# Kernel tuning notes

Measured on AMD Instinct MI355X. Metric: run time of the kernel, lower is better.

The kernel has to match this reference:

```python
import jax, jax.numpy as jnp
import numpy as np

NEG_SLOPE = 0.01  # torch nn.LeakyReLU default


def setup_inputs() -> dict:
    key = jax.random.key(0)
    k1, k2, k3, k4 = jax.random.split(key, 4)
    B, N, d = 256, 64, 64
    embeddings = jax.random.normal(k1, (B, N, d), dtype=jnp.float32)
    # nn.Linear(em_dim, em_dim): weight [d, d] (out, in), bias [d]
    w_W = jax.random.normal(k2, (d, d), dtype=jnp.float32) / np.sqrt(d)
    w_b = jax.random.normal(k3, (d,), dtype=jnp.float32) * 0.01
    # nn.Linear(em_dim, 1): weight [1, d] -> stored as [d], bias [1]
    a_W = jax.random.normal(k4, (d,), dtype=jnp.float32) / np.sqrt(d)
    a_b = jnp.zeros((1,), dtype=jnp.float32)
    return {"embeddings": embeddings, "w_W": w_W, "w_b": w_b, "a_W": a_W, "a_b": a_b}


def reference(embeddings, w_W, w_b, a_W, a_b):
    # pairwise elementwise product: value[b,i,j,d] = emb[b,i,d] * emb[b,j,d]
    value = embeddings[:, :, None, :] * embeddings[:, None, :, :]  # [B,N,N,d]
    # small linear d->d (torch Linear: x @ W.T + b)
    qk = jnp.einsum('bijd,ed->bije', value, w_W) + w_b
    qk = jnp.where(qk >= 0, qk, NEG_SLOPE * qk)  # LeakyReLU
    # dropout is identity in eval mode
    logits = jnp.einsum('bijd,d->bij', qk, a_W) + a_b[0]  # linear d->1, squeeze
    alphas = jax.nn.softmax(logits, axis=-1)[..., None]  # [B,N,N,1]
    return alphas, value
```

## Files before the change

kernel.cpp:

```cpp
#include <hip/hip_runtime.h>

typedef __attribute__((ext_vector_type(8))) short short8;
typedef __attribute__((ext_vector_type(4))) float floatx4;
typedef __attribute__((ext_vector_type(4))) int   intx4;

#define NEG_SLOPE 0.01f

__device__ __forceinline__ short f2bf(float f) {
    unsigned u = __float_as_uint(f);
    unsigned r = (u + 0x7FFFu + ((u >> 16) & 1u)) >> 16;
    return (short)r;
}

__device__ __forceinline__ int pack2(float x, float y) {
    return (int)(unsigned short)f2bf(x) | ((int)(unsigned short)f2bf(y) << 16);
}

__global__ __launch_bounds__(256, 2)
void afm_kernel(const float* __restrict__ emb,
                const float* __restrict__ wW,
                const float* __restrict__ wb,
                const float* __restrict__ aW,
                float* __restrict__ aOut,
                float* __restrict__ vOut) {
    __shared__ __align__(16) float sEf[64][68];
    __shared__ __align__(16) float sW [64][68];
    __shared__ __align__(16) short sEb[64][72];
    __shared__ __align__(16) float sei[4][64];
    __shared__ __align__(16) float swb[64];
    __shared__ __align__(16) float saw[64];
    __shared__ __align__(16) float slog[4][64];

    const int tid   = threadIdx.x;
    const int lane  = tid & 63;
    const int w     = tid >> 6;
    const int blk   = blockIdx.x;
    const int b     = blk >> 4;
    const int iBase = (blk & 15) << 2;
    const int i     = iBase + w;

    const float* embB = emb + (size_t)b * 4096;

    {
        int row = tid >> 2;
        int c0  = (tid & 3) << 4;
        const float* src = embB + row * 64 + c0;
        float4 a0 = *(const float4*)(src);
        float4 a1 = *(const float4*)(src + 4);
        float4 a2 = *(const float4*)(src + 8);
        float4 a3 = *(const float4*)(src + 12);
        *(float4*)&sEf[row][c0]      = a0;
        *(float4*)&sEf[row][c0 + 4]  = a1;
        *(float4*)&sEf[row][c0 + 8]  = a2;
        *(float4*)&sEf[row][c0 + 12] = a3;
        intx4 q0, q1;
        q0[0] = pack2(a0.x, a0.y); q0[1] = pack2(a0.z, a0.w);
        q0[2] = pack2(a1.x, a1.y); q0[3] = pack2(a1.z, a1.w);
        q1[0] = pack2(a2.x, a2.y); q1[1] = pack2(a2.z, a2.w);
        q1[2] = pack2(a3.x, a3.y); q1[3] = pack2(a3.z, a3.w);
        *(intx4*)&sEb[row][c0]     = q0;
        *(intx4*)&sEb[row][c0 + 8] = q1;

        const float* wsrc = wW + row * 64 + c0;
        float4 b0 = *(const float4*)(wsrc);
        float4 b1 = *(const float4*)(wsrc + 4);
        float4 b2 = *(const float4*)(wsrc + 8);
        float4 b3 = *(const float4*)(wsrc + 12);
        *(float4*)&sW[row][c0]      = b0;
        *(float4*)&sW[row][c0 + 4]  = b1;
        *(float4*)&sW[row][c0 + 8]  = b2;
        *(float4*)&sW[row][c0 + 12] = b3;

        sei[w][lane] = embB[i * 64 + lane];
        if (tid < 64)        swb[tid]       = wb[tid];
        else if (tid < 128)  saw[tid - 64]  = aW[tid - 64];
    }
    __syncthreads();

    {
        float* base = vOut + ((size_t)(b * 64 + i) << 12);
        const int joff = lane >> 4;
        const int d0   = (lane & 15) << 2;
        float4 ei = *(float4*)&sei[w][d0];
        #pragma unroll
        for (int c = 0; c < 16; ++c) {
            int j = (c << 2) + joff;
            float4 ej = *(float4*)&sEf[j][d0];
            float4 v;
            v.x = ei.x * ej.x; v.y = ei.y * ej.y;
            v.z = ei.z * ej.z; v.w = ei.w * ej.w;
            *(float4*)(base + (c << 8) + (lane << 2)) = v;
        }
    }

    const int lo = lane & 15, hi = lane >> 4;
    floatx4 acc[4][4];
    #pragma unroll
    for (int jt = 0; jt < 4; ++jt)
        #pragma unroll
        for (int et = 0; et < 4; ++et)
            acc[jt][et] = (floatx4){0.f, 0.f, 0.f, 0.f};

    #pragma unroll
    for (int kt = 0; kt < 2; ++kt) {
        const int d0 = kt * 32 + hi * 8;
        float4 ei0 = *(float4*)&sei[w][d0];
        float4 ei1 = *(float4*)&sei[w][d0 + 4];
        short8 bf[4];
        #pragma unroll
        for (int et = 0; et < 4; ++et) {
            int e = et * 16 + lo;
            float4 w0 = *(float4*)&sW[e][d0];
            float4 w1 = *(float4*)&sW[e][d0 + 4];
            short8 t;
            t[0] = f2bf(w0.x * ei0.x); t[1] = f2bf(w0.y * ei0.y);
            t[2] = f2bf(w0.z * ei0.z); t[3] = f2bf(w0.w * ei0.w);
            t[4] = f2bf(w1.x * ei1.x); t[5] = f2bf(w1.y * ei1.y);
            t[6] = f2bf(w1.z * ei1.z); t[7] = f2bf(w1.w * ei1.w);
            bf[et] = t;
        }
        #pragma unroll
        for (int jt = 0; jt < 4; ++jt) {
            short8 af = *(short8*)&sEb[jt * 16 + lo][d0];
            #pragma unroll
            for (int et = 0; et < 4; ++et)
                acc[jt][et] = __builtin_amdgcn_mfma_f32_16x16x32_bf16(
                    af, bf[et], acc[jt][et], 0, 0, 0);
        }
    }

    float wbv[4], awv[4];
    #pragma unroll
    for (int et = 0; et < 4; ++et) {
        int e = et * 16 + lo;
        wbv[et] = swb[e];
        awv[et] = saw[e];
    }

    float lg[16];
    #pragma unroll
    for (int jt = 0; jt < 4; ++jt) {
        #pragma unroll
        for (int r = 0; r < 4; ++r) {
            float p = 0.f;
            #pragma unroll
            for (int et = 0; et < 4; ++et) {
                float x = acc[jt][et][r] + wbv[et];
                x = (x >= 0.f) ? x : NEG_SLOPE * x;
                p += awv[et] * x;
            }
            p += __shfl_xor(p, 1);
            p += __shfl_xor(p, 2);
            p += __shfl_xor(p, 4);
            p += __shfl_xor(p, 8);
            lg[jt * 4 + r] = p;
        }
    }

    float m = lg[0];
    #pragma unroll
    for (int k = 1; k < 16; ++k) m = fmaxf(m, lg[k]);
    m = fmaxf(m, __shfl_xor(m, 16));
    m = fmaxf(m, __shfl_xor(m, 32));

    float ex[16];
    float s = 0.f;
    #pragma unroll
    for (int k = 0; k < 16; ++k) { ex[k] = __expf(lg[k] - m); s += ex[k]; }
    s += __shfl_xor(s, 16);
    s += __shfl_xor(s, 32);
    float inv = 1.f / s;

    if (lo == 0) {
        #pragma unroll
        for (int jt = 0; jt < 4; ++jt)
            #pragma unroll
            for (int r = 0; r < 4; ++r)
                slog[w][jt * 16 + hi * 4 + r] = ex[jt * 4 + r] * inv;
    }
    __syncthreads();
    aOut[((size_t)(b * 64 + i) << 6) + lane] = slog[w][lane];
}

extern "C" void kernel_launch(void* const* d_in, const int* in_sizes, int n_in,
                              void* d_out, int out_size, void* d_ws, size_t ws_size,
                              hipStream_t stream) {
    const float* emb = (const float*)d_in[0];
    const float* wW  = (const float*)d_in[1];
    const float* wb  = (const float*)d_in[2];
    const float* aW  = (const float*)d_in[3];
    float* aOut = (float*)d_out;
    float* vOut = aOut + (size_t)256 * 64 * 64;
    afm_kernel<<<4096, 256, 0, stream>>>(emb, wW, wb, aW, aOut, vOut);
}
```

Baseline: 285.1 us.

## Drop LDS staging, read operands from global, use nontemporal value stores

Removes the shared-memory staging of embeddings, weights and biases. Operands are now read straight from global memory, relying on the caches, and bf16 fragments are packed in registers. The large value tensor is written with nontemporal stores, and the launch bound is raised to 4 blocks per CU. The final block barrier becomes a compiler-only fence, since each wave reads back only its own LDS row. This aims to cut LDS traffic, barrier stalls and LDS-limited occupancy, at the cost of redundant global loads per wave.

```diff
diff --git a/kernel.cpp b/kernel.cpp
--- a/kernel.cpp
+++ b/kernel.cpp
@@ -2,98 +2,57 @@
 
 typedef __attribute__((ext_vector_type(8))) short short8;
 typedef __attribute__((ext_vector_type(4))) float floatx4;
-typedef __attribute__((ext_vector_type(4))) int   intx4;
 
 #define NEG_SLOPE 0.01f
 
-__device__ __forceinline__ short f2bf(float f) {
+__device__ __forceinline__ unsigned bfr(float f) {
     unsigned u = __float_as_uint(f);
-    unsigned r = (u + 0x7FFFu + ((u >> 16) & 1u)) >> 16;
-    return (short)r;
+    return (u + 0x7FFFu + ((u >> 16) & 1u)) >> 16;
+}
+__device__ __forceinline__ int pack2(float x, float y) {
+    return (int)bfr(x) | (int)(bfr(y) << 16);
+}
+__device__ __forceinline__ short8 packfrag(float4 a, float4 b) {
+    union { int i[4]; short8 s; } u;
+    u.i[0] = pack2(a.x, a.y); u.i[1] = pack2(a.z, a.w);
+    u.i[2] = pack2(b.x, b.y); u.i[3] = pack2(b.z, b.w);
+    return u.s;
 }
 
-__device__ __forceinline__ int pack2(float x, float y) {
-    return (int)(unsigned short)f2bf(x) | ((int)(unsigned short)f2bf(y) << 16);
-}
-
-__global__ __launch_bounds__(256, 2)
+__global__ __launch_bounds__(256, 4)
 void afm_kernel(const float* __restrict__ emb,
                 const float* __restrict__ wW,
                 const float* __restrict__ wb,
                 const float* __restrict__ aW,
                 float* __restrict__ aOut,
                 float* __restrict__ vOut) {
-    __shared__ __align__(16) float sEf[64][68];
-    __shared__ __align__(16) float sW [64][68];
-    __shared__ __align__(16) short sEb[64][72];
-    __shared__ __align__(16) float sei[4][64];
-    __shared__ __align__(16) float swb[64];
-    __shared__ __align__(16) float saw[64];
-    __shared__ __align__(16) float slog[4][64];
+    __shared__ float slog[4][64];
 
-    const int tid   = threadIdx.x;
-    const int lane  = tid & 63;
-    const int w     = tid >> 6;
-    const int blk   = blockIdx.x;
-    const int b     = blk >> 4;
-    const int iBase = (blk & 15) << 2;
-    const int i     = iBase + w;
+    const int tid  = threadIdx.x;
+    const int lane = tid & 63;
+    const int w    = tid >> 6;
+    const int lo   = lane & 15;
+    const int hi   = lane >> 4;
+    const int blk  = blockIdx.x;
+    const int b    = blk >> 4;
+    const int i    = ((blk & 15) << 2) + w;
 
-    const float* embB = emb + (size_t)b * 4096;
+    const float* embB   = emb + ((size_t)b << 12);
+    const float* ei_row = embB + (i << 6);
 
     {
-        int row = tid >> 2;
-        int c0  = (tid & 3) << 4;
-        const float* src = embB + row * 64 + c0;
-        float4 a0 = *(const float4*)(src);
-        float4 a1 = *(const float4*)(src + 4);
-        float4 a2 = *(const float4*)(src + 8);
-        float4 a3 = *(const float4*)(src + 12);
-        *(float4*)&sEf[row][c0]      = a0;
-        *(float4*)&sEf[row][c0 + 4]  = a1;
-        *(float4*)&sEf[row][c0 + 8]  = a2;
-        *(float4*)&sEf[row][c0 + 12] = a3;
-        intx4 q0, q1;
-        q0[0] = pack2(a0.x, a0.y); q0[1] = pack2(a0.z, a0.w);
-        q0[2] = pack2(a1.x, a1.y); q0[3] = pack2(a1.z, a1.w);
-        q1[0] = pack2(a2.x, a2.y); q1[1] = pack2(a2.z, a2.w);
-        q1[2] = pack2(a3.x, a3.y); q1[3] = pack2(a3.z, a3.w);
-        *(intx4*)&sEb[row][c0]     = q0;
-        *(intx4*)&sEb[row][c0 + 8] = q1;
-
-        const float* wsrc = wW + row * 64 + c0;
-        float4 b0 = *(const float4*)(wsrc);
-        float4 b1 = *(const float4*)(wsrc + 4);
-        float4 b2 = *(const float4*)(wsrc + 8);
-        float4 b3 = *(const float4*)(wsrc + 12);
-        *(float4*)&sW[row][c0]      = b0;
-        *(float4*)&sW[row][c0 + 4]  = b1;
-        *(float4*)&sW[row][c0 + 8]  = b2;
-        *(float4*)&sW[row][c0 + 12] = b3;
-
-        sei[w][lane] = embB[i * 64 + lane];
-        if (tid < 64)        swb[tid]       = wb[tid];
-        else if (tid < 128)  saw[tid - 64]  = aW[tid - 64];
-    }
-    __syncthreads();
-
-    {
-        float* base = vOut + ((size_t)(b * 64 + i) << 12);
-        const int joff = lane >> 4;
-        const int d0   = (lane & 15) << 2;
-        float4 ei = *(float4*)&sei[w][d0];
+        float4 ei = *(const float4*)(ei_row + (lo << 2));
+        float* base = vOut + (((size_t)((b << 6) + i)) << 12) + (lane << 2);
         #pragma unroll
         for (int c = 0; c < 16; ++c) {
-            int j = (c << 2) + joff;
-            float4 ej = *(float4*)&sEf[j][d0];
-            float4 v;
-            v.x = ei.x * ej.x; v.y = ei.y * ej.y;
-            v.z = ei.z * ej.z; v.w = ei.w * ej.w;
-            *(float4*)(base + (c << 8) + (lane << 2)) = v;
+            float4 ej = *(const float4*)(embB + ((((c << 2) + hi)) << 6) + (lo << 2));
+            floatx4 v;
+            v[0] = ei.x * ej.x; v[1] = ei.y * ej.y;
+            v[2] = ei.z * ej.z; v[3] = ei.w * ej.w;
+            __builtin_nontemporal_store(v, (floatx4*)(base + (c << 8)));
         }
     }
 
-    const int lo = lane & 15, hi = lane >> 4;
     floatx4 acc[4][4];
     #pragma unroll
     for (int jt = 0; jt < 4; ++jt)
@@ -103,38 +62,40 @@
 
     #pragma unroll
     for (int kt = 0; kt < 2; ++kt) {
-        const int d0 = kt * 32 + hi * 8;
-        float4 ei0 = *(float4*)&sei[w][d0];
-        float4 ei1 = *(float4*)&sei[w][d0 + 4];
-        short8 bf[4];
+        const int d0 = (kt << 5) + (hi << 3);
+        float4 ei0 = *(const float4*)(ei_row + d0);
+        float4 ei1 = *(const float4*)(ei_row + d0 + 4);
+        short8 bfrag[4];
         #pragma unroll
         for (int et = 0; et < 4; ++et) {
-            int e = et * 16 + lo;
-            float4 w0 = *(float4*)&sW[e][d0];
-            float4 w1 = *(float4*)&sW[e][d0 + 4];
-            short8 t;
-            t[0] = f2bf(w0.x * ei0.x); t[1] = f2bf(w0.y * ei0.y);
-            t[2] = f2bf(w0.z * ei0.z); t[3] = f2bf(w0.w * ei0.w);
-            t[4] = f2bf(w1.x * ei1.x); t[5] = f2bf(w1.y * ei1.y);
-            t[6] = f2bf(w1.z * ei1.z); t[7] = f2bf(w1.w * ei1.w);
-            bf[et] = t;
+            const float* pw = wW + ((((et << 4) + lo)) << 6) + d0;
+            float4 w0 = *(const float4*)(pw);
+            float4 w1 = *(const float4*)(pw + 4);
+            float4 p0, p1;
+            p0.x = w0.x * ei0.x; p0.y = w0.y * ei0.y;
+            p0.z = w0.z * ei0.z; p0.w = w0.w * ei0.w;
+            p1.x = w1.x * ei1.x; p1.y = w1.y * ei1.y;
+            p1.z = w1.z * ei1.z; p1.w = w1.w * ei1.w;
+            bfrag[et] = packfrag(p0, p1);
         }
         #pragma unroll
         for (int jt = 0; jt < 4; ++jt) {
-            short8 af = *(short8*)&sEb[jt * 16 + lo][d0];
+            const float* pe = embB + ((((jt << 4) + lo)) << 6) + d0;
+            float4 a0 = *(const float4*)(pe);
+            float4 a1 = *(const float4*)(pe + 4);
+            short8 afrag = packfrag(a0, a1);
             #pragma unroll
             for (int et = 0; et < 4; ++et)
                 acc[jt][et] = __builtin_amdgcn_mfma_f32_16x16x32_bf16(
-                    af, bf[et], acc[jt][et], 0, 0, 0);
+                    afrag, bfrag[et], acc[jt][et], 0, 0, 0);
         }
     }
 
     float wbv[4], awv[4];
     #pragma unroll
     for (int et = 0; et < 4; ++et) {
-        int e = et * 16 + lo;
-        wbv[et] = swb[e];
-        awv[et] = saw[e];
+        wbv[et] = wb[(et << 4) + lo];
+        awv[et] = aW[(et << 4) + lo];
     }
 
     float lg[16];
@@ -178,8 +139,8 @@
             for (int r = 0; r < 4; ++r)
                 slog[w][jt * 16 + hi * 4 + r] = ex[jt * 4 + r] * inv;
     }
-    __syncthreads();
-    aOut[((size_t)(b * 64 + i) << 6) + lane] = slog[w][lane];
+    asm volatile("" ::: "memory");
+    aOut[(((size_t)((b << 6) + i)) << 6) + lane] = slog[w][lane];
 }
 
 extern "C" void kernel_launch(void* const* d_in, const int* in_sizes, int n_in,
```

New measurement: 329.8 us. 15.7% more time.
